# Kernel optimization log

Measured on AMD Instinct MI355X. Metric: run time of the kernel, lower is better.

## Reference

```python
import jax, jax.numpy as jnp
import numpy as np

N, E, H, L, B = 200000, 800000, 128, 4, 2000  # nodes, directed edges, hidden, layers, graphs
ATOM, BOND = 28, 6


def setup_inputs() -> dict:
    key = jax.random.key(0)
    ks = jax.random.split(key, 12)
    h = jax.random.normal(ks[0], (N, ATOM), jnp.float32)
    e = jax.random.normal(ks[1], (E, BOND), jnp.float32)
    # paired directed edges: edge 2i = (u->v), edge 2i+1 = (v->u), so rev(k) = k ^ 1
    u = jax.random.randint(ks[2], (E // 2,), 0, N)
    v = jax.random.randint(ks[3], (E // 2,), 0, N)
    src = jnp.stack([u, v], axis=1).reshape(-1)
    dst = jnp.stack([v, u], axis=1).reshape(-1)
    graph_id = jnp.sort(jax.random.randint(ks[4], (N,), 0, B))
    s = 1.0 / np.sqrt(H).astype(np.float32)
    W_emb = jax.random.normal(ks[5], (ATOM, H), jnp.float32) * (1.0 / np.sqrt(ATOM))
    W_init = jax.random.normal(ks[6], (H + BOND, H), jnp.float32) * s
    b_init = jnp.zeros((H,), jnp.float32)
    W_layers = jax.random.normal(ks[7], (L, H, H), jnp.float32) * s
    b_layers = jnp.zeros((L, H), jnp.float32)
    W_ro = jax.random.normal(ks[8], (H, H), jnp.float32) * s
    W_pred = jax.random.normal(ks[9], (H, 1), jnp.float32) * s
    b_pred = jnp.zeros((1,), jnp.float32)
    snorm_n = jnp.ones((N, 1), jnp.float32)
    snorm_e = jnp.ones((E, 1), jnp.float32)
    return dict(h=h, e=e, W_emb=W_emb, W_init=W_init, b_init=b_init,
                W_layers=W_layers, b_layers=b_layers, W_ro=W_ro,
                W_pred=W_pred, b_pred=b_pred, src=src, dst=dst,
                graph_id=graph_id, snorm_n=snorm_n, snorm_e=snorm_e)


def reference(h, e, W_emb, W_init, b_init, W_layers, b_layers, W_ro,
              W_pred, b_pred, src, dst, graph_id, snorm_n, snorm_e):
    n_nodes = h.shape[0]
    n_edges = src.shape[0]
    rev = jnp.arange(n_edges) ^ 1  # paired reverse-edge index
    # node embedding (dropout is identity at p=0); x kept as residual input per source
    x = h @ W_emb  # [N, H]
    # init_message_func: per-edge relu(Linear(cat(h_src, e)))
    he = jax.nn.relu(jnp.concatenate([x[src], e], axis=1) @ W_init + b_init)  # [E, H]
    # D-MPNN layers: aggregate incoming edge states at src node, exclude reverse edge,
    # linear + relu (norms disabled in this config), outer residual add
    n_layers = W_layers.shape[0]
    for l in range(n_layers):
        agg = jax.ops.segment_sum(he, dst, num_segments=n_nodes)  # sum of edge states into each node
        m = agg[src] - he[rev]                                    # exclude reverse edge
        he = jax.nn.relu(m @ W_layers[l] + b_layers[l]) + he      # residual
    # update_all(copy_edge, sum): node state = sum of incoming edge states
    h_out = jax.ops.segment_sum(he, dst, num_segments=n_nodes)  # [N, H]
    h_ro = h_out @ W_ro                                          # linear_ro (no bias)
    # readout == 'sum': per-graph sum of node states
    hg = jax.ops.segment_sum(h_ro, graph_id, num_segments=B)     # [B, H]
    return hg @ W_pred + b_pred                                  # [B, 1]
```

## Files before the change

### kernel.cpp

```cpp
#include <hip/hip_runtime.h>
#include <hip/hip_bf16.h>

#define H 128
#define ATOM 28
#define BOND 6
#define NLAYERS 4
#define TE 32
#define LW 136
#define LKI 72
typedef unsigned short US;
typedef unsigned int UI;
typedef short bf16x8 __attribute__((ext_vector_type(8)));
typedef float f32x4 __attribute__((ext_vector_type(4)));
#define MFMA(a,b,c) __builtin_amdgcn_mfma_f32_16x16x32_bf16((a),(b),(c),0,0,0)

__device__ __forceinline__ float bf2f(US u) {
    union { unsigned int i; float f; } v; v.i = ((unsigned int)u) << 16; return v.f;
}
__device__ __forceinline__ US f2bf(float f) {
    union { float f; unsigned int i; } v; v.f = f;
    unsigned int r = v.i + 0x7FFF + ((v.i >> 16) & 1);
    return (US)(r >> 16);
}
__device__ __forceinline__ float in_ld(const void* p, long long i, int bf) {
    return bf ? bf2f(((const US*)p)[i]) : ((const float*)p)[i];
}

__global__ void detect_kernel(const void* snorm, int* flag) {
    const US* u = (const US*)snorm;
    *flag = (u[0] == 0x3F80 && u[2] == 0x3F80) ? 1 : 0;
}

__global__ void fail_kernel(void* out, int nB, float val, const int* flag) {
    int i = blockIdx.x * 256 + threadIdx.x;
    if (i < nB) {
        if (*flag) ((US*)out)[i] = f2bf(val);
        else       ((float*)out)[i] = val;
    }
}

__global__ void build_wt(const void* __restrict__ W_emb, const void* __restrict__ W_init,
                         const int* __restrict__ flag, US* __restrict__ WtG) {
    int bf = *flag;
    int k = blockIdx.x;
    int c = threadIdx.x;
    float v = 0.f;
    if (k < ATOM) {
        for (int j = 0; j < H; ++j)
            v += in_ld(W_emb, k * H + j, bf) * in_ld(W_init, (long long)j * H + c, bf);
    } else if (k < ATOM + BOND) {
        v = in_ld(W_init, (long long)(H + k - ATOM) * H + c, bf);
    }
    WtG[c * 64 + k] = f2bf(v);
}

__global__ void build_wtL(const void* __restrict__ W_layers, const int* __restrict__ flag,
                          US* __restrict__ WtL) {
    int bf = *flag;
    int l = blockIdx.x >> 7, n = blockIdx.x & 127;
    int k = threadIdx.x;
    long long si = (long long)l * H * H + (long long)k * H + n;
    WtL[((long long)l * H + n) * H + k] = bf ? ((const US*)W_layers)[si]
                                             : f2bf(((const float*)W_layers)[si]);
}

__global__ void build_wp(const void* __restrict__ W_ro, const void* __restrict__ W_pred,
                         const int* __restrict__ flag, float* __restrict__ wp) {
    int bf = *flag;
    int c = threadIdx.x;
    float s = 0.f;
    for (int j = 0; j < H; ++j)
        s += in_ld(W_ro, (long long)c * H + j, bf) * in_ld(W_pred, j, bf);
    wp[c] = s;
}

__global__ void hist_kernel(const int* __restrict__ dst, int* __restrict__ cnt, int nE) {
    int k = blockIdx.x * 256 + threadIdx.x;
    if (k < nE) atomicAdd(&cnt[dst[k]], 1);
}

__global__ __launch_bounds__(256) void scan1(const int* __restrict__ cnt,
                                             int* __restrict__ rowptr,
                                             int* __restrict__ partials, int nN) {
    __shared__ int sd[256];
    int t = threadIdx.x;
    int base = blockIdx.x * 1024 + t * 4;
    int l0 = (base + 0 < nN) ? cnt[base + 0] : 0;
    int l1 = (base + 1 < nN) ? cnt[base + 1] : 0;
    int l2 = (base + 2 < nN) ? cnt[base + 2] : 0;
    int l3 = (base + 3 < nN) ? cnt[base + 3] : 0;
    int s = l0 + l1 + l2 + l3;
    sd[t] = s; __syncthreads();
    for (int off = 1; off < 256; off <<= 1) {
        int v = (t >= off) ? sd[t - off] : 0;
        __syncthreads();
        sd[t] += v;
        __syncthreads();
    }
    int excl = sd[t] - s;
    if (base + 0 < nN) rowptr[base + 0] = excl;
    if (base + 1 < nN) rowptr[base + 1] = excl + l0;
    if (base + 2 < nN) rowptr[base + 2] = excl + l0 + l1;
    if (base + 3 < nN) rowptr[base + 3] = excl + l0 + l1 + l2;
    if (t == 255) partials[blockIdx.x] = sd[255];
}

__global__ __launch_bounds__(256) void scan2(const int* __restrict__ partials,
                                             int* __restrict__ blockoff, int SB) {
    __shared__ int sd[256];
    int t = threadIdx.x;
    int v = (t < SB) ? partials[t] : 0;
    sd[t] = v; __syncthreads();
    for (int off = 1; off < 256; off <<= 1) {
        int x = (t >= off) ? sd[t - off] : 0;
        __syncthreads();
        sd[t] += x;
        __syncthreads();
    }
    blockoff[t] = sd[t] - v;
}

__global__ void scan3(int* __restrict__ rowptr, int* __restrict__ cursor,
                      const int* __restrict__ blockoff, int nN, int nE) {
    int i = blockIdx.x * 256 + threadIdx.x;
    if (i < nN) {
        int v = rowptr[i] + blockoff[i >> 10];
        rowptr[i] = v;
        cursor[i] = v;
    }
    if (i == 0) rowptr[nN] = nE;
}

__global__ void fill_kernel(const int* __restrict__ dst, int* __restrict__ cursor,
                            int* __restrict__ ein, int nE) {
    int k = blockIdx.x * 256 + threadIdx.x;
    if (k < nE) {
        int pos = atomicAdd(&cursor[dst[k]], 1);
        ein[pos] = k;
    }
}

__global__ __launch_bounds__(256) void agg_gather(
    const US* __restrict__ he, const int* __restrict__ rowptr,
    const int* __restrict__ ein, US* __restrict__ agg, int nN) {
    int n = blockIdx.x * 4 + (threadIdx.x >> 6);
    int lane = threadIdx.x & 63;
    if (n >= nN) return;
    const UI* heU = (const UI*)he;
    int s = rowptr[n], epos = rowptr[n + 1];
    float f0 = 0.f, f1 = 0.f;
    int idx = s;
    for (; idx + 4 <= epos; idx += 4) {
        int e0 = ein[idx], e1 = ein[idx + 1], e2 = ein[idx + 2], e3 = ein[idx + 3];
        UI u0 = heU[(long long)e0 * 64 + lane];
        UI u1 = heU[(long long)e1 * 64 + lane];
        UI u2 = heU[(long long)e2 * 64 + lane];
        UI u3 = heU[(long long)e3 * 64 + lane];
        f0 += bf2f((US)(u0 & 0xFFFF)) + bf2f((US)(u1 & 0xFFFF))
            + bf2f((US)(u2 & 0xFFFF)) + bf2f((US)(u3 & 0xFFFF));
        f1 += bf2f((US)(u0 >> 16)) + bf2f((US)(u1 >> 16))
            + bf2f((US)(u2 >> 16)) + bf2f((US)(u3 >> 16));
    }
    for (; idx < epos; ++idx) {
        UI u = heU[(long long)ein[idx] * 64 + lane];
        f0 += bf2f((US)(u & 0xFFFF));
        f1 += bf2f((US)(u >> 16));
    }
    ((UI*)agg)[(long long)n * 64 + lane] = (UI)f2bf(f0) | ((UI)f2bf(f1) << 16);
}

__global__ __launch_bounds__(256) void readout_dot(
    const US* __restrict__ he, const int* __restrict__ rowptr,
    const int* __restrict__ ein, const float* __restrict__ wp,
    const int* __restrict__ graph_id, float* __restrict__ hgS, int nN) {
    __shared__ float sv[4];
    __shared__ int sg[4];
    int wave = threadIdx.x >> 6, lane = threadIdx.x & 63;
    int n = blockIdx.x * 4 + wave;
    bool valid = n < nN;
    float w0 = wp[2 * lane], w1 = wp[2 * lane + 1];
    float v = 0.f;
    if (valid) {
        const UI* heU = (const UI*)he;
        int s = rowptr[n], epos = rowptr[n + 1];
        float f0 = 0.f, f1 = 0.f;
        int idx = s;
        for (; idx + 4 <= epos; idx += 4) {
            int e0 = ein[idx], e1 = ein[idx + 1], e2 = ein[idx + 2], e3 = ein[idx + 3];
            UI u0 = heU[(long long)e0 * 64 + lane];
            UI u1 = heU[(long long)e1 * 64 + lane];
            UI u2 = heU[(long long)e2 * 64 + lane];
            UI u3 = heU[(long long)e3 * 64 + lane];
            f0 += bf2f((US)(u0 & 0xFFFF)) + bf2f((US)(u1 & 0xFFFF))
                + bf2f((US)(u2 & 0xFFFF)) + bf2f((US)(u3 & 0xFFFF));
            f1 += bf2f((US)(u0 >> 16)) + bf2f((US)(u1 >> 16))
                + bf2f((US)(u2 >> 16)) + bf2f((US)(u3 >> 16));
        }
        for (; idx < epos; ++idx) {
            UI u = heU[(long long)ein[idx] * 64 + lane];
            f0 += bf2f((US)(u & 0xFFFF));
            f1 += bf2f((US)(u >> 16));
        }
        v = f0 * w0 + f1 * w1;
        #pragma unroll
        for (int off = 32; off > 0; off >>= 1) v += __shfl_down(v, off);
    }
    if (lane == 0) {
        sv[wave] = valid ? v : 0.f;
        sg[wave] = valid ? graph_id[n] : -1;
    }
    __syncthreads();
    if (threadIdx.x == 0) {
        int cg = sg[0]; float acc = sv[0];
        #pragma unroll
        for (int w = 1; w < 4; ++w) {
            if (sg[w] == cg) acc += sv[w];
            else {
                if (cg >= 0) unsafeAtomicAdd(&hgS[cg], acc);
                cg = sg[w]; acc = sv[w];
            }
        }
        if (cg >= 0) unsafeAtomicAdd(&hgS[cg], acc);
    }
}

__global__ __launch_bounds__(256) void agg_dot(
    const US* __restrict__ agg, const float* __restrict__ wp,
    const int* __restrict__ graph_id, float* __restrict__ hgS, int nN) {
    __shared__ float sv[4];
    __shared__ int sg[4];
    int wave = threadIdx.x >> 6, lane = threadIdx.x & 63;
    int n = blockIdx.x * 4 + wave;
    bool valid = n < nN;
    float v = 0.f;
    if (valid) {
        UI u = ((const UI*)agg)[(long long)n * 64 + lane];
        v = bf2f((US)(u & 0xFFFF)) * wp[2 * lane]
          + bf2f((US)(u >> 16)) * wp[2 * lane + 1];
        #pragma unroll
        for (int off = 32; off > 0; off >>= 1) v += __shfl_down(v, off);
    }
    if (lane == 0) {
        sv[wave] = valid ? v : 0.f;
        sg[wave] = valid ? graph_id[n] : -1;
    }
    __syncthreads();
    if (threadIdx.x == 0) {
        int cg = sg[0]; float acc = sv[0];
        #pragma unroll
        for (int w = 1; w < 4; ++w) {
            if (sg[w] == cg) acc += sv[w];
            else {
                if (cg >= 0) unsafeAtomicAdd(&hgS[cg], acc);
                cg = sg[w]; acc = sv[w];
            }
        }
        if (cg >= 0) unsafeAtomicAdd(&hgS[cg], acc);
    }
}

__global__ void finish_kernel(const float* __restrict__ hgS, const void* __restrict__ b_pred,
                              const int* __restrict__ flag, void* __restrict__ out, int nB) {
    int bf = *flag;
    int i = blockIdx.x * 256 + threadIdx.x;
    if (i < nB) {
        float r = hgS[i] + in_ld(b_pred, 0, bf);
        if (bf) ((US*)out)[i] = f2bf(r);
        else    ((float*)out)[i] = r;
    }
}

__global__ __launch_bounds__(256) void scatter_cas(
    const US* __restrict__ he, const int* __restrict__ dst,
    US* __restrict__ agg, long long totalPairs) {
    const UI* heU = (const UI*)he;
    UI* aggU = (UI*)agg;
    long long i = (long long)blockIdx.x * blockDim.x + threadIdx.x;
    long long stride = (long long)gridDim.x * blockDim.x;
    for (; i < totalPairs; i += stride) {
        int k = (int)(i >> 6);
        int jp = (int)(i & 63);
        UI pv = heU[i];
        float v0 = bf2f((US)(pv & 0xFFFF));
        float v1 = bf2f((US)(pv >> 16));
        UI* addr = aggU + (long long)dst[k] * 64 + jp;
        UI old = *addr, assumed;
        do {
            assumed = old;
            UI nv = (UI)f2bf(bf2f((US)(assumed & 0xFFFF)) + v0)
                  | ((UI)f2bf(bf2f((US)(assumed >> 16)) + v1) << 16);
            old = atomicCAS(addr, assumed, nv);
        } while (old != assumed);
    }
}

__global__ __launch_bounds__(256) void mfma_init(
    const void* __restrict__ h, const void* __restrict__ e,
    const US* __restrict__ WtG, const void* __restrict__ b_init,
    const int* __restrict__ src, const int* __restrict__ flag,
    US* __restrict__ he, int nE) {
    __shared__ __align__(16) US sA[TE * LKI];
    const int bf = *flag;
    const int tid = threadIdx.x;
    const int wave = tid >> 6, lane = tid & 63;
    const int quad = lane >> 4, l16 = lane & 15;
    const int ncol0 = wave * 32;
    float rb0 = in_ld(b_init, ncol0 + l16, bf);
    float rb1 = in_ld(b_init, ncol0 + 16 + l16, bf);
    bf16x8 bw[2][2];
    #pragma unroll
    for (int i = 0; i < 2; ++i)
        #pragma unroll
        for (int c = 0; c < 2; ++c)
            bw[i][c] = *(const bf16x8*)&WtG[(ncol0 + c * 16 + l16) * 64 + i * 32 + quad * 8];

    const int r = tid >> 3, u0 = (tid & 7) * 4;
    int ntiles = nE / TE;
    for (int t = blockIdx.x; t < ntiles; t += gridDim.x) {
        int k0 = t * TE;
        __syncthreads();
        {
            int k = k0 + r;
            int s = src[k];
            UI* dU = (UI*)&sA[r * LKI];
            if (bf) {
                const UI* hU = (const UI*)h;
                const UI* eU = (const UI*)e;
                #pragma unroll
                for (int q = 0; q < 4; ++q) {
                    int idx = u0 + q;
                    UI v = 0;
                    if (idx < 14) v = hU[(long long)s * 14 + idx];
                    else if (idx < 17) v = eU[(long long)k * 3 + (idx - 14)];
                    dU[idx] = v;
                }
            } else {
                const float* hF = (const float*)h;
                const float* eF = (const float*)e;
                #pragma unroll
                for (int q = 0; q < 4; ++q) {
                    int idx = u0 + q;
                    int c0 = idx * 2, c1 = idx * 2 + 1;
                    float f0 = 0.f, f1 = 0.f;
                    if (c0 < ATOM) f0 = hF[(long long)s * ATOM + c0];
                    else if (c0 < ATOM + BOND) f0 = eF[(long long)k * BOND + (c0 - ATOM)];
                    if (c1 < ATOM) f1 = hF[(long long)s * ATOM + c1];
                    else if (c1 < ATOM + BOND) f1 = eF[(long long)k * BOND + (c1 - ATOM)];
                    dU[idx] = (UI)f2bf(f0) | ((UI)f2bf(f1) << 16);
                }
            }
        }
        __syncthreads();

        f32x4 acc00 = {0,0,0,0}, acc01 = {0,0,0,0}, acc10 = {0,0,0,0}, acc11 = {0,0,0,0};
        #pragma unroll
        for (int i = 0; i < 2; ++i) {
            int kb = i * 32 + quad * 8;
            bf16x8 a0 = *(const bf16x8*)&sA[l16 * LKI + kb];
            bf16x8 a1 = *(const bf16x8*)&sA[(l16 + 16) * LKI + kb];
            acc00 = MFMA(a0, bw[i][0], acc00);
            acc01 = MFMA(a0, bw[i][1], acc01);
            acc10 = MFMA(a1, bw[i][0], acc10);
            acc11 = MFMA(a1, bw[i][1], acc11);
        }
        #pragma unroll
        for (int mt = 0; mt < 2; ++mt)
            #pragma unroll
            for (int reg = 0; reg < 4; ++reg) {
                int row = mt * 16 + quad * 4 + reg;
                long long hbase = (long long)(k0 + row) * H;
                #pragma unroll
                for (int nt = 0; nt < 2; ++nt) {
                    float a = mt ? (nt ? acc11[reg] : acc10[reg])
                                 : (nt ? acc01[reg] : acc00[reg]);
                    int col = ncol0 + nt * 16 + l16;
                    he[hbase + col] = f2bf(fmaxf(a + (nt ? rb1 : rb0), 0.f));
                }
            }
    }
}

__global__ __launch_bounds__(256) void mfma_layer(
    const US* __restrict__ agg, const int* __restrict__ src,
    const US* __restrict__ WtL, const void* __restrict__ b_layers,
    int layer, const int* __restrict__ flag, US* __restrict__ he, int nE) {
    __shared__ __align__(16) US sHe[2][TE * LW];
    __shared__ __align__(16) US sAgg[2][TE * LW];
    const int bf = *flag;
    const int tid = threadIdx.x;
    const int wave = tid >> 6, lane = tid & 63;
    const int quad = lane >> 4, l16 = lane & 15;
    const int ncol0 = wave * 32;
    float rb0 = in_ld(b_layers, (long long)layer * H + ncol0 + l16, bf);
    float rb1 = in_ld(b_layers, (long long)layer * H + ncol0 + 16 + l16, bf);
    const US* Wl = WtL + (size_t)layer * H * H;
    bf16x8 bw[4][2];
    #pragma unroll
    for (int i = 0; i < 4; ++i)
        #pragma unroll
        for (int c = 0; c < 2; ++c)
            bw[i][c] = *(const bf16x8*)&Wl[(ncol0 + c * 16 + l16) * H + i * 32 + quad * 8];

    const int r0 = tid >> 4, q0 = tid & 15;
    int ntiles = nE / TE;
    int t = blockIdx.x;
    uint4 vh0, vh1, va0, va1;
    if (t < ntiles) {
        int k0 = t * TE;
        const uint4* heG = (const uint4*)(he + (long long)k0 * H);
        vh0 = heG[tid]; vh1 = heG[tid + 256];
        int s0 = src[k0 + r0], s1 = src[k0 + r0 + 16];
        va0 = ((const uint4*)(agg + (long long)s0 * H))[q0];
        va1 = ((const uint4*)(agg + (long long)s1 * H))[q0];
    }
    int buf = 0;
    for (; t < ntiles; t += gridDim.x, buf ^= 1) {
        int k0 = t * TE;
        *(uint4*)&sHe[buf][r0 * LW + q0 * 8] = vh0;
        *(uint4*)&sHe[buf][(r0 + 16) * LW + q0 * 8] = vh1;
        *(uint4*)&sAgg[buf][r0 * LW + q0 * 8] = va0;
        *(uint4*)&sAgg[buf][(r0 + 16) * LW + q0 * 8] = va1;
        __syncthreads();
        int tn = t + gridDim.x;
        if (tn < ntiles) {
            int kn = tn * TE;
            const uint4* heG = (const uint4*)(he + (long long)kn * H);
            vh0 = heG[tid]; vh1 = heG[tid + 256];
            int s0 = src[kn + r0], s1 = src[kn + r0 + 16];
            va0 = ((const uint4*)(agg + (long long)s0 * H))[q0];
            va1 = ((const uint4*)(agg + (long long)s1 * H))[q0];
        }

        f32x4 g1a = {0,0,0,0}, g1b = {0,0,0,0}, g1c = {0,0,0,0}, g1d = {0,0,0,0};
        f32x4 g2a = {0,0,0,0}, g2b = {0,0,0,0}, g2c = {0,0,0,0}, g2d = {0,0,0,0};
        #pragma unroll
        for (int i = 0; i < 4; ++i) {
            int kb = i * 32 + quad * 8;
            bf16x8 aA0 = *(const bf16x8*)&sAgg[buf][l16 * LW + kb];
            bf16x8 aA1 = *(const bf16x8*)&sAgg[buf][(l16 + 16) * LW + kb];
            bf16x8 aH0 = *(const bf16x8*)&sHe[buf][l16 * LW + kb];
            bf16x8 aH1 = *(const bf16x8*)&sHe[buf][(l16 + 16) * LW + kb];
            g1a = MFMA(aA0, bw[i][0], g1a); g1b = MFMA(aA0, bw[i][1], g1b);
            g1c = MFMA(aA1, bw[i][0], g1c); g1d = MFMA(aA1, bw[i][1], g1d);
            g2a = MFMA(aH0, bw[i][0], g2a); g2b = MFMA(aH0, bw[i][1], g2b);
            g2c = MFMA(aH1, bw[i][0], g2c); g2d = MFMA(aH1, bw[i][1], g2d);
        }
        __syncthreads();

        #pragma unroll
        for (int mt = 0; mt < 2; ++mt)
            #pragma unroll
            for (int reg = 0; reg < 4; ++reg) {
                int row = mt * 16 + quad * 4 + reg;
                #pragma unroll
                for (int nt = 0; nt < 2; ++nt) {
                    float g1 = mt ? (nt ? g1d[reg] : g1c[reg])
                                  : (nt ? g1b[reg] : g1a[reg]);
                    float g2 = mt ? (nt ? g2d[reg ^ 1] : g2c[reg ^ 1])
                                  : (nt ? g2b[reg ^ 1] : g2a[reg ^ 1]);
                    int col = ncol0 + nt * 16 + l16;
                    float v = fmaxf(g1 - g2 + (nt ? rb1 : rb0), 0.f)
                            + bf2f(sHe[buf][row * LW + col]);
                    sAgg[buf][row * LW + col] = f2bf(v);
                }
            }
        int row2 = lane >> 1, half = lane & 1;
        int cbase = ncol0 + half * 16;
        uint4 o0 = *(const uint4*)&sAgg[buf][row2 * LW + cbase];
        uint4 o1 = *(const uint4*)&sAgg[buf][row2 * LW + cbase + 8];
        uint4* dst4 = (uint4*)(he + (long long)(k0 + row2) * H + cbase);
        dst4[0] = o0; dst4[1] = o1;
    }
}

extern "C" void kernel_launch(void* const* d_in, const int* in_sizes, int n_in,
                              void* d_out, int out_size, void* d_ws, size_t ws_size,
                              hipStream_t stream) {
    const void* h        = d_in[0];
    const void* e        = d_in[1];
    const void* W_emb    = d_in[2];
    const void* W_init   = d_in[3];
    const void* b_init   = d_in[4];
    const void* W_layers = d_in[5];
    const void* b_layers = d_in[6];
    const void* W_ro     = d_in[7];
    const void* W_pred   = d_in[8];
    const void* b_pred   = d_in[9];
    const int*  src      = (const int*)d_in[10];
    const int*  dst      = (const int*)d_in[11];
    const int*  graph_id = (const int*)d_in[12];
    const void* snorm_n  = d_in[13];

    int nN = in_sizes[0] / ATOM;
    int nE = in_sizes[1] / BOND;
    int nB = out_size;
    int SB = (nN + 1023) / 1024;

    size_t off = 0;
    auto alloc = [&](size_t bytes) { size_t o = off; off = (off + bytes + 255) & ~(size_t)255; return o; };
    size_t o_flag = alloc(256);
    size_t o_wt   = alloc((size_t)H * 64 * sizeof(US));
    size_t o_wtL  = alloc((size_t)NLAYERS * H * H * sizeof(US));
    size_t o_wp   = alloc((size_t)H * sizeof(float));
    size_t o_hgs  = alloc((size_t)nB * sizeof(float));
    size_t o_cnt  = alloc((size_t)nN * sizeof(int));
    size_t o_rp   = alloc((size_t)(nN + 1) * sizeof(int));
    size_t o_cur  = alloc((size_t)nN * sizeof(int));
    size_t o_par  = alloc(256 * sizeof(int));
    size_t o_boff = alloc(256 * sizeof(int));
    size_t o_ein  = alloc((size_t)nE * sizeof(int));
    size_t o_agg  = alloc((size_t)nN * H * sizeof(US));
    size_t o_he   = alloc((size_t)nE * H * sizeof(US));
    size_t needG  = off;

    char* W = (char*)d_ws;
    int*   flag   = (int*)(W + o_flag);
    US*    WtG    = (US*)(W + o_wt);
    US*    WtL    = (US*)(W + o_wtL);
    float* wp     = (float*)(W + o_wp);
    float* hgS    = (float*)(W + o_hgs);
    int*   cnt    = (int*)(W + o_cnt);
    int*   rowptr = (int*)(W + o_rp);
    int*   cursor = (int*)(W + o_cur);
    int*   part   = (int*)(W + o_par);
    int*   boff   = (int*)(W + o_boff);
    int*   ein    = (int*)(W + o_ein);
    US*    agg    = (US*)(W + o_agg);
    US*    he     = (US*)(W + o_he);

    detect_kernel<<<1, 1, 0, stream>>>(snorm_n, flag);
    build_wt<<<64, 128, 0, stream>>>(W_emb, W_init, flag, WtG);
    build_wtL<<<NLAYERS * H, 128, 0, stream>>>(W_layers, flag, WtL);
    build_wp<<<1, 128, 0, stream>>>(W_ro, W_pred, flag, wp);

    if (ws_size >= needG && SB <= 256) {
        hipMemsetAsync(cnt, 0, (size_t)nN * sizeof(int), stream);
        hist_kernel<<<(nE + 255) / 256, 256, 0, stream>>>(dst, cnt, nE);
        scan1<<<SB, 256, 0, stream>>>(cnt, rowptr, part, nN);
        scan2<<<1, 256, 0, stream>>>(part, boff, SB);
        scan3<<<(nN + 255) / 256, 256, 0, stream>>>(rowptr, cursor, boff, nN, nE);
        fill_kernel<<<(nE + 255) / 256, 256, 0, stream>>>(dst, cursor, ein, nE);

        mfma_init<<<2048, 256, 0, stream>>>(h, e, WtG, b_init, src, flag, he, nE);
        for (int l = 0; l < NLAYERS; ++l) {
            agg_gather<<<(nN + 3) / 4, 256, 0, stream>>>(he, rowptr, ein, agg, nN);
            mfma_layer<<<2048, 256, 0, stream>>>(agg, src, WtL, b_layers, l, flag, he, nE);
        }
        hipMemsetAsync(hgS, 0, (size_t)nB * sizeof(float), stream);
        readout_dot<<<(nN + 3) / 4, 256, 0, stream>>>(he, rowptr, ein, wp, graph_id, hgS, nN);
        finish_kernel<<<(nB + 255) / 256, 256, 0, stream>>>(hgS, b_pred, flag, d_out, nB);
        return;
    }

    size_t off2 = 0;
    auto alloc2 = [&](size_t bytes) { size_t o = off2; off2 = (off2 + bytes + 255) & ~(size_t)255; return o; };
    alloc2(256);
    alloc2((size_t)H * 64 * sizeof(US));
    alloc2((size_t)NLAYERS * H * H * sizeof(US));
    size_t f2_wp  = alloc2((size_t)H * sizeof(float));
    size_t f2_hgs = alloc2((size_t)nB * sizeof(float));
    size_t f2_agg = alloc2((size_t)nN * H * sizeof(US));
    size_t f2_he  = alloc2((size_t)nE * H * sizeof(US));
    size_t needT  = off2;

    if (ws_size >= needT) {
        float* wp2  = (float*)(W + f2_wp);
        float* hgS2 = (float*)(W + f2_hgs);
        US*    agg2 = (US*)(W + f2_agg);
        US*    he2  = (US*)(W + f2_he);
        build_wp<<<1, 128, 0, stream>>>(W_ro, W_pred, flag, wp2);
        mfma_init<<<2048, 256, 0, stream>>>(h, e, WtG, b_init, src, flag, he2, nE);
        for (int l = 0; l < NLAYERS; ++l) {
            hipMemsetAsync(agg2, 0, (size_t)nN * H * sizeof(US), stream);
            scatter_cas<<<2048, 256, 0, stream>>>(he2, dst, agg2, (long long)nE * (H / 2));
            mfma_layer<<<2048, 256, 0, stream>>>(agg2, src, WtL, b_layers, l, flag, he2, nE);
        }
        hipMemsetAsync(agg2, 0, (size_t)nN * H * sizeof(US), stream);
        scatter_cas<<<2048, 256, 0, stream>>>(he2, dst, agg2, (long long)nE * (H / 2));
        hipMemsetAsync(hgS2, 0, (size_t)nB * sizeof(float), stream);
        agg_dot<<<(nN + 3) / 4, 256, 0, stream>>>(agg2, wp2, graph_id, hgS2, nN);
        finish_kernel<<<(nB + 255) / 256, 256, 0, stream>>>(hgS2, b_pred, flag, d_out, nB);
    } else {
        float val = (float)(ws_size >> 20) * 1e6f;
        fail_kernel<<<(nB + 255) / 256, 256, 0, stream>>>(d_out, nB, val, flag);
    }
}
```

Measured before the change: 1.112 ms.

## Split init message into per-node GEMM plus per-edge bond GEMM

Result: no change. 1.124 ms (+1.1%).

```diff
diff --git a/kernel.cpp b/kernel.cpp
--- a/kernel.cpp
+++ b/kernel.cpp
@@ -8,6 +8,7 @@
 #define TE 32
 #define LW 136
 #define LKI 72
+#define LE 40
 typedef unsigned short US;
 typedef unsigned int UI;
 typedef short bf16x8 __attribute__((ext_vector_type(8)));
@@ -48,10 +49,17 @@
     if (k < ATOM) {
         for (int j = 0; j < H; ++j)
             v += in_ld(W_emb, k * H + j, bf) * in_ld(W_init, (long long)j * H + c, bf);
-    } else if (k < ATOM + BOND) {
-        v = in_ld(W_init, (long long)(H + k - ATOM) * H + c, bf);
     }
     WtG[c * 64 + k] = f2bf(v);
+}
+
+__global__ void build_w2x(const void* __restrict__ W_init, const int* __restrict__ flag,
+                          US* __restrict__ W2x) {
+    int bf = *flag;
+    int k = blockIdx.x;
+    int c = threadIdx.x;
+    float v = (k < BOND) ? in_ld(W_init, (long long)(H + k) * H + c, bf) : 0.f;
+    W2x[c * 32 + k] = f2bf(v);
 }
 
 __global__ void build_wtL(const void* __restrict__ W_layers, const int* __restrict__ flag,
@@ -294,19 +302,16 @@
     }
 }
 
-__global__ __launch_bounds__(256) void mfma_init(
-    const void* __restrict__ h, const void* __restrict__ e,
-    const US* __restrict__ WtG, const void* __restrict__ b_init,
-    const int* __restrict__ src, const int* __restrict__ flag,
-    US* __restrict__ he, int nE) {
+__global__ __launch_bounds__(256) void node_gemm(
+    const void* __restrict__ h, const US* __restrict__ WtG,
+    const int* __restrict__ flag, US* __restrict__ xn, int nN) {
     __shared__ __align__(16) US sA[TE * LKI];
+    __shared__ __align__(16) US sO[TE * LW];
     const int bf = *flag;
     const int tid = threadIdx.x;
     const int wave = tid >> 6, lane = tid & 63;
     const int quad = lane >> 4, l16 = lane & 15;
     const int ncol0 = wave * 32;
-    float rb0 = in_ld(b_init, ncol0 + l16, bf);
-    float rb1 = in_ld(b_init, ncol0 + 16 + l16, bf);
     bf16x8 bw[2][2];
     #pragma unroll
     for (int i = 0; i < 2; ++i)
@@ -314,41 +319,25 @@
         for (int c = 0; c < 2; ++c)
             bw[i][c] = *(const bf16x8*)&WtG[(ncol0 + c * 16 + l16) * 64 + i * 32 + quad * 8];
 
-    const int r = tid >> 3, u0 = (tid & 7) * 4;
-    int ntiles = nE / TE;
+    UI* sAU = (UI*)sA;
+    for (int i = tid; i < TE * (LKI / 2); i += 256) sAU[i] = 0u;
+
+    int ntiles = (nN + TE - 1) / TE;
     for (int t = blockIdx.x; t < ntiles; t += gridDim.x) {
-        int k0 = t * TE;
-        __syncthreads();
-        {
-            int k = k0 + r;
-            int s = src[k];
-            UI* dU = (UI*)&sA[r * LKI];
-            if (bf) {
-                const UI* hU = (const UI*)h;
-                const UI* eU = (const UI*)e;
-                #pragma unroll
-                for (int q = 0; q < 4; ++q) {
-                    int idx = u0 + q;
-                    UI v = 0;
-                    if (idx < 14) v = hU[(long long)s * 14 + idx];
-                    else if (idx < 17) v = eU[(long long)k * 3 + (idx - 14)];
-                    dU[idx] = v;
-                }
-            } else {
-                const float* hF = (const float*)h;
-                const float* eF = (const float*)e;
-                #pragma unroll
-                for (int q = 0; q < 4; ++q) {
-                    int idx = u0 + q;
-                    int c0 = idx * 2, c1 = idx * 2 + 1;
-                    float f0 = 0.f, f1 = 0.f;
-                    if (c0 < ATOM) f0 = hF[(long long)s * ATOM + c0];
-                    else if (c0 < ATOM + BOND) f0 = eF[(long long)k * BOND + (c0 - ATOM)];
-                    if (c1 < ATOM) f1 = hF[(long long)s * ATOM + c1];
-                    else if (c1 < ATOM + BOND) f1 = eF[(long long)k * BOND + (c1 - ATOM)];
-                    dU[idx] = (UI)f2bf(f0) | ((UI)f2bf(f1) << 16);
+        int n0 = t * TE;
+        __syncthreads();
+        for (int i = tid; i < TE * 14; i += 256) {
+            int r = i / 14, u = i % 14;
+            int n = n0 + r;
+            UI v = 0;
+            if (n < nN) {
+                if (bf) v = ((const UI*)h)[(long long)n * 14 + u];
+                else {
+                    const float* hF = (const float*)h + (long long)n * ATOM + 2 * u;
+                    v = (UI)f2bf(hF[0]) | ((UI)f2bf(hF[1]) << 16);
                 }
             }
+            sAU[r * (LKI / 2) + u] = v;
         }
         __syncthreads();
 
@@ -368,15 +357,100 @@
             #pragma unroll
             for (int reg = 0; reg < 4; ++reg) {
                 int row = mt * 16 + quad * 4 + reg;
-                long long hbase = (long long)(k0 + row) * H;
+                #pragma unroll
+                for (int nt = 0; nt < 2; ++nt) {
+                    float a = mt ? (nt ? acc11[reg] : acc10[reg])
+                                 : (nt ? acc01[reg] : acc00[reg]);
+                    sO[row * LW + ncol0 + nt * 16 + l16] = f2bf(a);
+                }
+            }
+        int row2 = lane >> 1, half = lane & 1;
+        int cbase = ncol0 + half * 16;
+        int n = n0 + row2;
+        if (n < nN) {
+            uint4 o0 = *(const uint4*)&sO[row2 * LW + cbase];
+            uint4 o1 = *(const uint4*)&sO[row2 * LW + cbase + 8];
+            uint4* dst4 = (uint4*)(xn + (long long)n * H + cbase);
+            dst4[0] = o0; dst4[1] = o1;
+        }
+    }
+}
+
+__global__ __launch_bounds__(256) void init_edge(
+    const void* __restrict__ e, const US* __restrict__ xn,
+    const US* __restrict__ W2x, const void* __restrict__ b_init,
+    const int* __restrict__ src, const int* __restrict__ flag,
+    US* __restrict__ he, int nE) {
+    __shared__ __align__(16) US sE[TE * LE];
+    __shared__ __align__(16) US sX[TE * LW];
+    const int bf = *flag;
+    const int tid = threadIdx.x;
+    const int wave = tid >> 6, lane = tid & 63;
+    const int quad = lane >> 4, l16 = lane & 15;
+    const int ncol0 = wave * 32;
+    float rb0 = in_ld(b_init, ncol0 + l16, bf);
+    float rb1 = in_ld(b_init, ncol0 + 16 + l16, bf);
+    bf16x8 bw2[2];
+    #pragma unroll
+    for (int c = 0; c < 2; ++c)
+        bw2[c] = *(const bf16x8*)&W2x[(ncol0 + c * 16 + l16) * 32 + quad * 8];
+
+    UI* sEU = (UI*)sE;
+    for (int i = tid; i < TE * (LE / 2); i += 256) sEU[i] = 0u;
+
+    int ntiles = nE / TE;
+    for (int t = blockIdx.x; t < ntiles; t += gridDim.x) {
+        int k0 = t * TE;
+        __syncthreads();
+        if (tid < TE * 3) {
+            int r = tid / 3, u = tid % 3;
+            UI v;
+            if (bf) v = ((const UI*)e)[(long long)(k0 + r) * 3 + u];
+            else {
+                const float* eF = (const float*)e + (long long)(k0 + r) * BOND + 2 * u;
+                v = (UI)f2bf(eF[0]) | ((UI)f2bf(eF[1]) << 16);
+            }
+            sEU[r * (LE / 2) + u] = v;
+        }
+        #pragma unroll
+        for (int ii = 0; ii < 2; ++ii) {
+            int i = tid + ii * 256;
+            int r = i >> 4, q = i & 15;
+            int s = src[k0 + r];
+            *(uint4*)&sX[r * LW + q * 8] = ((const uint4*)(xn + (long long)s * H))[q];
+        }
+        __syncthreads();
+
+        f32x4 acc00 = {0,0,0,0}, acc01 = {0,0,0,0}, acc10 = {0,0,0,0}, acc11 = {0,0,0,0};
+        {
+            int kb = quad * 8;
+            bf16x8 a0 = *(const bf16x8*)&sE[l16 * LE + kb];
+            bf16x8 a1 = *(const bf16x8*)&sE[(l16 + 16) * LE + kb];
+            acc00 = MFMA(a0, bw2[0], acc00);
+            acc01 = MFMA(a0, bw2[1], acc01);
+            acc10 = MFMA(a1, bw2[0], acc10);
+            acc11 = MFMA(a1, bw2[1], acc11);
+        }
+        #pragma unroll
+        for (int mt = 0; mt < 2; ++mt)
+            #pragma unroll
+            for (int reg = 0; reg < 4; ++reg) {
+                int row = mt * 16 + quad * 4 + reg;
                 #pragma unroll
                 for (int nt = 0; nt < 2; ++nt) {
                     float a = mt ? (nt ? acc11[reg] : acc10[reg])
                                  : (nt ? acc01[reg] : acc00[reg]);
                     int col = ncol0 + nt * 16 + l16;
-                    he[hbase + col] = f2bf(fmaxf(a + (nt ? rb1 : rb0), 0.f));
+                    float v = fmaxf(a + bf2f(sX[row * LW + col]) + (nt ? rb1 : rb0), 0.f);
+                    sX[row * LW + col] = f2bf(v);
                 }
             }
+        int row2 = lane >> 1, half = lane & 1;
+        int cbase = ncol0 + half * 16;
+        uint4 o0 = *(const uint4*)&sX[row2 * LW + cbase];
+        uint4 o1 = *(const uint4*)&sX[row2 * LW + cbase + 8];
+        uint4* dst4 = (uint4*)(he + (long long)(k0 + row2) * H + cbase);
+        dst4[0] = o0; dst4[1] = o1;
     }
 }
 
@@ -500,6 +574,7 @@
     auto alloc = [&](size_t bytes) { size_t o = off; off = (off + bytes + 255) & ~(size_t)255; return o; };
     size_t o_flag = alloc(256);
     size_t o_wt   = alloc((size_t)H * 64 * sizeof(US));
+    size_t o_w2x  = alloc((size_t)H * 32 * sizeof(US));
     size_t o_wtL  = alloc((size_t)NLAYERS * H * H * sizeof(US));
     size_t o_wp   = alloc((size_t)H * sizeof(float));
     size_t o_hgs  = alloc((size_t)nB * sizeof(float));
@@ -516,6 +591,7 @@
     char* W = (char*)d_ws;
     int*   flag   = (int*)(W + o_flag);
     US*    WtG    = (US*)(W + o_wt);
+    US*    W2x    = (US*)(W + o_w2x);
     US*    WtL    = (US*)(W + o_wtL);
     float* wp     = (float*)(W + o_wp);
     float* hgS    = (float*)(W + o_hgs);
@@ -530,6 +606,7 @@
 
     detect_kernel<<<1, 1, 0, stream>>>(snorm_n, flag);
     build_wt<<<64, 128, 0, stream>>>(W_emb, W_init, flag, WtG);
+    build_w2x<<<32, 128, 0, stream>>>(W_init, flag, W2x);
     build_wtL<<<NLAYERS * H, 128, 0, stream>>>(W_layers, flag, WtL);
     build_wp<<<1, 128, 0, stream>>>(W_ro, W_pred, flag, wp);
 
@@ -541,7 +618,8 @@
         scan3<<<(nN + 255) / 256, 256, 0, stream>>>(rowptr, cursor, boff, nN, nE);
         fill_kernel<<<(nE + 255) / 256, 256, 0, stream>>>(dst, cursor, ein, nE);
 
-        mfma_init<<<2048, 256, 0, stream>>>(h, e, WtG, b_init, src, flag, he, nE);
+        node_gemm<<<2048, 256, 0, stream>>>(h, WtG, flag, agg , nN);
+        init_edge<<<2048, 256, 0, stream>>>(e, agg , W2x, b_init, src, flag, he, nE);
         for (int l = 0; l < NLAYERS; ++l) {
             agg_gather<<<(nN + 3) / 4, 256, 0, stream>>>(he, rowptr, ein, agg, nN);
             mfma_layer<<<2048, 256, 0, stream>>>(agg, src, WtL, b_layers, l, flag, he, nE);
@@ -556,6 +634,7 @@
     auto alloc2 = [&](size_t bytes) { size_t o = off2; off2 = (off2 + bytes + 255) & ~(size_t)255; return o; };
     alloc2(256);
     alloc2((size_t)H * 64 * sizeof(US));
+    alloc2((size_t)H * 32 * sizeof(US));
     alloc2((size_t)NLAYERS * H * H * sizeof(US));
     size_t f2_wp  = alloc2((size_t)H * sizeof(float));
     size_t f2_hgs = alloc2((size_t)nB * sizeof(float));
@@ -569,7 +648,8 @@
         US*    agg2 = (US*)(W + f2_agg);
         US*    he2  = (US*)(W + f2_he);
         build_wp<<<1, 128, 0, stream>>>(W_ro, W_pred, flag, wp2);
-        mfma_init<<<2048, 256, 0, stream>>>(h, e, WtG, b_init, src, flag, he2, nE);
+        node_gemm<<<2048, 256, 0, stream>>>(h, WtG, flag, agg2 , nN);
+        init_edge<<<2048, 256, 0, stream>>>(e, agg2, W2x, b_init, src, flag, he2, nE);
         for (int l = 0; l < NLAYERS; ++l) {
             hipMemsetAsync(agg2, 0, (size_t)nN * H * sizeof(US), stream);
             scatter_cas<<<2048, 256, 0, stream>>>(he2, dst, agg2, (long long)nE * (H / 2));
```
